# Kernel tuning notes

Hardware: AMD Instinct MI355X
Metric: run time of the kernel (lower is better)

## Reference

```python
import jax, jax.numpy as jnp
import numpy as np

N, C_IN, C_OUT, K_CHEB, BATCH = 2048, 64, 64, 4, 8


def setup_inputs() -> dict:
    key = jax.random.key(0)
    k1, k2, k3, k4, k5 = jax.random.split(key, 5)
    # Xavier-uniform-like scales
    s_nn = float(np.sqrt(6.0 / (N + N)))
    s_th = float(np.sqrt(6.0 / (C_IN + C_OUT)))
    return {
        "X": jax.random.normal(k1, (BATCH, N, C_IN), dtype=jnp.float32),
        "Ws": jax.random.uniform(k2, (N, N), jnp.float32, -s_nn, s_nn),
        "W_alpha": jax.random.uniform(k3, (N, N), jnp.float32, -s_nn, s_nn),
        "Theta_s": jax.random.uniform(k4, (K_CHEB, C_IN, C_OUT), jnp.float32, -s_th, s_th),
        "Theta_d": jax.random.uniform(k5, (K_CHEB, C_IN, C_OUT), jnp.float32, -s_th, s_th),
    }


def reference(X, Ws, W_alpha, Theta_s, Theta_d):
    B, n, c_in = X.shape
    K = Theta_s.shape[0]

    # ---- static filter: sum_k (T_k(Ws) @ X) @ Theta_s[k] ----
    # T_0 = I, so T_0 @ X = X
    static_filter = jnp.einsum('bni,io->bno', X, Theta_s[0])
    if K > 1:
        T_prev2 = jnp.eye(n, dtype=X.dtype)
        T_prev1 = Ws  # T_1
        for k in range(1, K):
            TkX = jnp.einsum('nm,bmi->bni', T_prev1, X)
            static_filter = static_filter + jnp.einsum('bni,io->bno', TkX, Theta_s[k])
            if k + 1 < K:  # incremental Chebyshev recursion (same values as from-scratch)
                T_prev2, T_prev1 = T_prev1, 2.0 * (Ws @ T_prev1) - T_prev2

    # ---- dynamic filter ----
    # Wd = X @ (W_alpha @ X)^T  -> [B, n, n]
    WaX = jnp.einsum('nm,bmi->bni', W_alpha, X)
    Wd = jnp.einsum('bni,bmi->bnm', X, WaX)

    dynamic_filter = jnp.einsum('bni,io->bno', X, Theta_d[0])
    if K > 1:
        Td_prev2 = jnp.broadcast_to(jnp.eye(n, dtype=X.dtype), (B, n, n))
        Td_prev1 = Wd  # T_1
        for k in range(1, K):
            TkX = jnp.einsum('bnm,bmi->bni', Td_prev1, X)
            dynamic_filter = dynamic_filter + jnp.einsum('bni,io->bno', TkX, Theta_d[k])
            if k + 1 < K:
                Td_prev2, Td_prev1 = Td_prev1, 2.0 * jnp.matmul(Wd, Td_prev1) - Td_prev2

    return jax.nn.relu(static_filter) + jax.nn.relu(dynamic_filter)
```

## Files before the change

### kernel.cpp

```cpp
#include <hip/hip_runtime.h>

typedef __attribute__((ext_vector_type(8))) short bf16x8;
typedef __attribute__((ext_vector_type(4))) float f32x4;

__device__ __forceinline__ ushort f32_to_bf16(float f) {
    union { float f; unsigned u; } v; v.f = f;
    unsigned b = v.u + 0x7FFF + ((v.u >> 16) & 1);
    return (ushort)(b >> 16);
}
__device__ __forceinline__ float bf16_to_f32(ushort h) {
    union { unsigned u; float f; } v; v.u = ((unsigned)h) << 16;
    return v.f;
}
__device__ __forceinline__ void split2(float x, ushort& a, ushort& b) {
    a = f32_to_bf16(x); float r1 = x - bf16_to_f32(a);
    b = f32_to_bf16(r1);
}

__device__ __forceinline__ void vmwait4() { asm volatile("s_waitcnt vmcnt(4)" ::: "memory"); }
__device__ __forceinline__ void vmwait0() { asm volatile("s_waitcnt vmcnt(0)" ::: "memory"); }
__device__ __forceinline__ void lgwait0() { asm volatile("s_waitcnt lgkmcnt(0)" ::: "memory"); }
__device__ __forceinline__ void blockbar() {
    __builtin_amdgcn_sched_barrier(0);
    __builtin_amdgcn_s_barrier();
    __builtin_amdgcn_sched_barrier(0);
}

__device__ __forceinline__ void stage64x64(const ushort* gsrc, int row_stride_elems,
                                           char* lds, int t256) {
    const char* gb = (const char*)gsrc;
    const int rs = row_stride_elems * 2;
#pragma unroll
    for (int j = 0; j < 2; ++j) {
        int o = (j * 256 + t256) * 16;
        int row = o >> 7;
        int col = (o & 127) ^ ((row & 7) << 4);
        __builtin_amdgcn_global_load_lds(
            (const __attribute__((address_space(1))) unsigned int*)(gb + row * rs + col),
            (__attribute__((address_space(3))) unsigned int*)(lds + o), 16, 0, 0);
    }
}

__device__ __forceinline__ bf16x8 fragld(const char* lds, int row, int kbyte) {
    return *(const bf16x8*)(lds + (row << 7) + (kbyte ^ ((row & 7) << 4)));
}

__global__ __launch_bounds__(256) void prep_all(const float* __restrict__ X,
        ushort* __restrict__ XT1, ushort* __restrict__ XT2,
        ushort* __restrict__ X1o, ushort* __restrict__ X2o,
        const float* __restrict__ Ws, ushort* __restrict__ Ws16,
        const float* __restrict__ Wa, ushort* __restrict__ Wa1, ushort* __restrict__ Wa2,
        const float* __restrict__ Ths, ushort* __restrict__ ThsT) {
    __shared__ float tile[64][68];
    const int bx = blockIdx.x;
    const int t = threadIdx.x;
    if (bx < 256) {
        const int b = bx >> 5, n0 = (bx & 31) * 64;
#pragma unroll
        for (int it = 0; it < 4; ++it) {
            int f = it * 256 + t, r = f >> 4, q = (f & 15) * 4;
            float4 v = *(const float4*)&X[((size_t)b * 2048 + n0 + r) * 64 + q];
            tile[r][q + 0] = v.x; tile[r][q + 1] = v.y; tile[r][q + 2] = v.z; tile[r][q + 3] = v.w;
        }
        __syncthreads();
#pragma unroll
        for (int it = 0; it < 4; ++it) {
            int f = it * 256 + t, c = f >> 4, q = (f & 15) * 4;
            ushort4 h1, h2;
            split2(tile[q + 0][c], h1.x, h2.x); split2(tile[q + 1][c], h1.y, h2.y);
            split2(tile[q + 2][c], h1.z, h2.z); split2(tile[q + 3][c], h1.w, h2.w);
            size_t a = (size_t)(b * 64 + c) * 2048 + n0 + q;
            *(ushort4*)&XT1[a] = h1; *(ushort4*)&XT2[a] = h2;
        }
#pragma unroll
        for (int it = 0; it < 4; ++it) {
            int f = it * 256 + t, n = f >> 4, q = (f & 15) * 4;
            ushort4 h1, h2;
            split2(tile[n][q + 0], h1.x, h2.x); split2(tile[n][q + 1], h1.y, h2.y);
            split2(tile[n][q + 2], h1.z, h2.z); split2(tile[n][q + 3], h1.w, h2.w);
            size_t a = (size_t)(n0 + n) * 512 + b * 64 + q;
            *(ushort4*)&X1o[a] = h1; *(ushort4*)&X2o[a] = h2;
        }
    } else if (bx < 2304) {
        size_t idx = ((size_t)(bx - 256) * 256 + t) * 8;
#pragma unroll
        for (int h = 0; h < 2; ++h) {
            float4 v = *(const float4*)&Ws[idx + h * 4];
            ushort4 a;
            a.x = f32_to_bf16(v.x); a.y = f32_to_bf16(v.y);
            a.z = f32_to_bf16(v.z); a.w = f32_to_bf16(v.w);
            *(ushort4*)&Ws16[idx + h * 4] = a;
        }
    } else if (bx < 4352) {
        size_t idx = ((size_t)(bx - 2304) * 256 + t) * 8;
#pragma unroll
        for (int h = 0; h < 2; ++h) {
            float4 v = *(const float4*)&Wa[idx + h * 4];
            ushort4 a, b;
            split2(v.x, a.x, b.x); split2(v.y, a.y, b.y);
            split2(v.z, a.z, b.z); split2(v.w, a.w, b.w);
            *(ushort4*)&Wa1[idx + h * 4] = a; *(ushort4*)&Wa2[idx + h * 4] = b;
        }
    } else {
        int idx = (bx - 4352) * 256 + t;
        int k = idx >> 12, o = (idx >> 6) & 63, i = idx & 63;
        ThsT[idx] = f32_to_bf16(Ths[k * 4096 + i * 64 + o]);
    }
}

template <int MODE>
__device__ __forceinline__ void gemm_s_body(int bx, const ushort* __restrict__ A,
        const ushort* __restrict__ BT, const ushort* __restrict__ CinT,
        ushort* __restrict__ YT, ushort* __restrict__ Yo, char* ls) {
    const int t = threadIdx.x;
    const int g = t >> 8, t256 = t & 255;
    const int m0 = (bx & 31) * 64, c0 = (bx >> 5) * 64;
    const int lane = t & 63;
    const int wg = (t >> 6) & 3, wr = wg >> 1, wc = wg & 1;
    const int l15 = lane & 15, l4 = lane >> 4;
    char* base = ls + g * 32768;
    const ushort* Ap = A + (size_t)m0 * 2048 + (size_t)g * 1024;
    const ushort* Bp = BT + (size_t)c0 * 2048 + (size_t)g * 1024;

    f32x4 z = {0.f, 0.f, 0.f, 0.f};
    f32x4 acc[2][2];
    acc[0][0] = z; acc[0][1] = z; acc[1][0] = z; acc[1][1] = z;

    stage64x64(Ap, 2048, base, t256);
    stage64x64(Bp, 2048, base + 8192, t256);
    for (int ts = 0; ts < 16; ++ts) {
        char* cur = base + (ts & 1) * 16384;
        if (ts < 15) {
            char* nxt = base + ((ts + 1) & 1) * 16384;
            stage64x64(Ap + (ts + 1) * 64, 2048, nxt, t256);
            stage64x64(Bp + (ts + 1) * 64, 2048, nxt + 8192, t256);
            vmwait4();
        } else {
            vmwait0();
        }
        blockbar();
#pragma unroll
        for (int s = 0; s < 2; ++s) {
            const int kb = s * 64 + l4 * 16;
            bf16x8 aF[2], bF[2];
#pragma unroll
            for (int f = 0; f < 2; ++f) {
                aF[f] = fragld(cur, wr * 32 + f * 16 + l15, kb);
                bF[f] = fragld(cur + 8192, wc * 32 + f * 16 + l15, kb);
            }
#pragma unroll
            for (int i = 0; i < 2; ++i)
#pragma unroll
                for (int j = 0; j < 2; ++j)
                    acc[i][j] = __builtin_amdgcn_mfma_f32_16x16x32_bf16(aF[i], bF[j], acc[i][j], 0, 0, 0);
        }
        lgwait0();
        blockbar();
    }

// ... 80 lines not shown
#pragma unroll
        for (int s = 0; s < 2; ++s) {
            const int kb = s * 64 + l4 * 16;
            bf16x8 aF[2], bF[2];
#pragma unroll
            for (int f = 0; f < 2; ++f) {
                aF[f] = fragld(cur, wr * 32 + f * 16 + l15, kb);
                bF[f] = fragld(cur + 8192, wc * 32 + f * 16 + l15, kb);
            }
#pragma unroll
            for (int i = 0; i < 2; ++i)
#pragma unroll
                for (int j = 0; j < 2; ++j)
                    acc[i][j] = __builtin_amdgcn_mfma_f32_16x16x32_bf16(aF[i], bF[j], acc[i][j], 0, 0, 0);
        }
        lgwait0();
        blockbar();
    }

    float* red = (float*)ls;
    float* tf = (float*)(ls + 17408);
    if (g == 0) {
#pragma unroll
        for (int i = 0; i < 2; ++i)
#pragma unroll
            for (int j = 0; j < 2; ++j) {
                const int lrb = wr * 32 + i * 16 + l4 * 4;
                const int lc = wc * 32 + j * 16 + l15;
#pragma unroll
                for (int r = 0; r < 4; ++r) red[(lrb + r) * 65 + lc] = acc[i][j][r];
            }
    }
    __syncthreads();
    if (g == 1) {
#pragma unroll
        for (int i = 0; i < 2; ++i)
#pragma unroll
            for (int j = 0; j < 2; ++j) {
                const int lrb = wr * 32 + i * 16 + l4 * 4;
                const int lc = wc * 32 + j * 16 + l15;
#pragma unroll
                for (int r = 0; r < 4; ++r) tf[(lrb + r) * 64 + lc] = red[(lrb + r) * 65 + lc] + acc[i][j][r];
            }
    }
    __syncthreads();
    {
        float* Pd = g2 ? P1 : P0;
        int row = t >> 3, q = (t & 7) * 8;
        *(float4*)&Pd[(size_t)(m0 + row) * 512 + c0 + q]     = *(float4*)&tf[row * 64 + q];
        *(float4*)&Pd[(size_t)(m0 + row) * 512 + c0 + q + 4] = *(float4*)&tf[row * 64 + q + 4];
    }
}

__device__ __forceinline__ void gemm3_body(int bx, const ushort* __restrict__ A1,
        const ushort* __restrict__ A2, const ushort* __restrict__ B1,
        const ushort* __restrict__ B2, float* __restrict__ WaXT, char* ls) {
    const int t = threadIdx.x;
    const int g = t >> 8, t256 = t & 255;
    const int m0 = (bx & 31) * 64, c0 = (bx >> 5) * 64;
    const int lane = t & 63;
    const int wg = (t >> 6) & 3, wr = wg >> 1, wc = wg & 1;
    const int l15 = lane & 15, l4 = lane >> 4;
    char* base = ls + g * 32768;
    const size_t kbase = (size_t)g * 1024;

    f32x4 z = {0.f, 0.f, 0.f, 0.f};
    f32x4 acc[2][2];
    acc[0][0] = z; acc[0][1] = z; acc[1][0] = z; acc[1][1] = z;

    for (int k0 = 0; k0 < 1024; k0 += 64) {
        stage64x64(A1 + (size_t)m0 * 2048 + kbase + k0, 2048, base + 0 * 8192, t256);
        stage64x64(A2 + (size_t)m0 * 2048 + kbase + k0, 2048, base + 1 * 8192, t256);
        stage64x64(B1 + (size_t)c0 * 2048 + kbase + k0, 2048, base + 2 * 8192, t256);
        stage64x64(B2 + (size_t)c0 * 2048 + kbase + k0, 2048, base + 3 * 8192, t256);
        __syncthreads();
#pragma unroll
        for (int s = 0; s < 2; ++s) {
            const int kb = s * 64 + l4 * 16;
            bf16x8 a1F[2], a2F[2], b1F[2], b2F[2];
#pragma unroll
            for (int f = 0; f < 2; ++f) {
                const int ar = wr * 32 + f * 16 + l15;
                const int br = wc * 32 + f * 16 + l15;
                a1F[f] = fragld(base + 0 * 8192, ar, kb);
                a2F[f] = fragld(base + 1 * 8192, ar, kb);
                b1F[f] = fragld(base + 2 * 8192, br, kb);
                b2F[f] = fragld(base + 3 * 8192, br, kb);
            }
#pragma unroll
            for (int i = 0; i < 2; ++i)
#pragma unroll
                for (int j = 0; j < 2; ++j) {
                    f32x4 a = acc[i][j];
                    a = __builtin_amdgcn_mfma_f32_16x16x32_bf16(a1F[i], b1F[j], a, 0, 0, 0);
                    a = __builtin_amdgcn_mfma_f32_16x16x32_bf16(a1F[i], b2F[j], a, 0, 0, 0);
                    a = __builtin_amdgcn_mfma_f32_16x16x32_bf16(a2F[i], b1F[j], a, 0, 0, 0);
                    acc[i][j] = a;
                }
        }
        __syncthreads();
    }

    float* red = (float*)ls;
    if (g == 0) {
#pragma unroll
        for (int i = 0; i < 2; ++i)
#pragma unroll
            for (int j = 0; j < 2; ++j) {
                const int lrb = wr * 32 + i * 16 + l4 * 4;
                const int lc = wc * 32 + j * 16 + l15;
#pragma unroll
                for (int r = 0; r < 4; ++r) red[(lrb + r) * 65 + lc] = acc[i][j][r];
            }
    }
    __syncthreads();
    if (g == 1) {
#pragma unroll
        for (int i = 0; i < 2; ++i)
#pragma unroll
            for (int j = 0; j < 2; ++j) {
                const int lrb = wr * 32 + i * 16 + l4 * 4;
                const int lc = wc * 32 + j * 16 + l15;
                f32x4 v;
#pragma unroll
                for (int r = 0; r < 4; ++r) v[r] = red[(lrb + r) * 65 + lc] + acc[i][j][r];
                *(f32x4*)&WaXT[(size_t)(c0 + lc) * 2048 + m0 + lrb] = v;
            }
    }
}

__device__ __forceinline__ void gram_body(int bx, const float* __restrict__ WaXT,
        const ushort* __restrict__ XT1, const ushort* __restrict__ XT2,
        float* __restrict__ Gpart, char* lsraw) {
    const int b = bx & 7, chunk = bx >> 3;
    float (*Lw)[68] = (float(*)[68])lsraw;
    float (*Rx)[68] = (float(*)[68])(lsraw + 64 * 68 * 4);
    const int t = threadIdx.x;
    const int n0 = chunk * 64;
    {
        const int r = t >> 3, q = (t & 7) * 8;
        size_t a = (size_t)(b * 64 + r) * 2048 + n0 + q;
        *(float4*)&Lw[r][q]     = *(const float4*)&WaXT[a];
        *(float4*)&Lw[r][q + 4] = *(const float4*)&WaXT[a + 4];
#pragma unroll
        for (int h = 0; h < 2; ++h) {
            ushort4 h1 = *(const ushort4*)&XT1[a + h * 4];
            ushort4 h2 = *(const ushort4*)&XT2[a + h * 4];
            Rx[r][q + h * 4 + 0] = bf16_to_f32(h1.x) + bf16_to_f32(h2.x);
            Rx[r][q + h * 4 + 1] = bf16_to_f32(h1.y) + bf16_to_f32(h2.y);
            Rx[r][q + h * 4 + 2] = bf16_to_f32(h1.z) + bf16_to_f32(h2.z);
            Rx[r][q + h * 4 + 3] = bf16_to_f32(h1.w) + bf16_to_f32(h2.w);
        }
    }
    __syncthreads();
    if (t < 256) {
        const int tx = t & 15, ty = t >> 4;
        float acc[4][4] = {{0.f,0.f,0.f,0.f},{0.f,0.f,0.f,0.f},{0.f,0.f,0.f,0.f},{0.f,0.f,0.f,0.f}};
        for (int n = 0; n < 64; ++n) {
            float a[4], bb[4];
#pragma unroll
            for (int i = 0; i < 4; ++i) { a[i] = Lw[ty * 4 + i][n]; bb[i] = Rx[tx * 4 + i][n]; }
#pragma unroll
            for (int i = 0; i < 4; ++i)
#pragma unroll
                for (int j = 0; j < 4; ++j) acc[i][j] = fmaf(a[i], bb[j], acc[i][j]);
        }
        float* gp = Gpart + (size_t)(chunk * 8 + b) * 4096;
#pragma unroll
        for (int i = 0; i < 4; ++i)
            *(float4*)&gp[(ty * 4 + i) * 64 + tx * 4] =
                make_float4(acc[i][0], acc[i][1], acc[i][2], acc[i][3]);
    }
}

__device__ __forceinline__ void cheb_body(int b, const float* __restrict__ Gpart,
        const float* __restrict__ Thd, ushort* __restrict__ DT1, ushort* __restrict__ DT2,
        char* lsraw) {
    float (*Gs)[68]  = (float(*)[68])lsraw;
    float (*C2s)[68] = (float(*)[68])(lsraw + 17408);
    float (*C3s)[68] = (float(*)[68])(lsraw + 34816);
    const int t = threadIdx.x;
    for (int i = t; i < 4096; i += 512) {
        float s = 0.f;
#pragma unroll
        for (int c = 0; c < 32; ++c) s += Gpart[((size_t)c * 8 + b) * 4096 + i];
        Gs[i >> 6][i & 63] = s;
    }
    __syncthreads();
    const int tx = t & 15, ty = (t >> 4) & 15;
    const int r0 = ty * 4, c0 = tx * 4;
    const bool act = t < 256;

    if (act) {
        float p[4][4] = {{0,0,0,0},{0,0,0,0},{0,0,0,0},{0,0,0,0}};
        for (int k = 0; k < 64; ++k) {
            float ar[4] = {Gs[r0][k], Gs[r0+1][k], Gs[r0+2][k], Gs[r0+3][k]};
            float4 bv = *(const float4*)&Gs[k][c0];
            float br[4] = {bv.x, bv.y, bv.z, bv.w};
#pragma unroll
            for (int i = 0; i < 4; ++i)
#pragma unroll
                for (int j = 0; j < 4; ++j) p[i][j] = fmaf(ar[i], br[j], p[i][j]);
        }
#pragma unroll
        for (int i = 0; i < 4; ++i)
#pragma unroll
            for (int j = 0; j < 4; ++j)
                C2s[r0+i][c0+j] = 2.f * p[i][j] - ((r0+i) == (c0+j) ? 1.f : 0.f);
    }
    __syncthreads();
    if (act) {
        float q[4][4] = {{0,0,0,0},{0,0,0,0},{0,0,0,0},{0,0,0,0}};
        for (int k = 0; k < 64; ++k) {
            float ar[4] = {Gs[r0][k], Gs[r0+1][k], Gs[r0+2][k], Gs[r0+3][k]};
            float4 bv = *(const float4*)&C2s[k][c0];
            float br[4] = {bv.x, bv.y, bv.z, bv.w};
#pragma unroll
            for (int i = 0; i < 4; ++i)
#pragma unroll
                for (int j = 0; j < 4; ++j) q[i][j] = fmaf(ar[i], br[j], q[i][j]);
        }
#pragma unroll
        for (int i = 0; i < 4; ++i)
#pragma unroll
            for (int j = 0; j < 4; ++j)
                C3s[r0+i][c0+j] = 2.f * q[i][j] - Gs[r0+i][c0+j];
    }
    __syncthreads();
    float d[4][4];
    if (act) {
#pragma unroll
        for (int i = 0; i < 4; ++i) {
            float4 t0 = *(const float4*)&Thd[(r0+i) * 64 + c0];
            d[i][0] = t0.x; d[i][1] = t0.y; d[i][2] = t0.z; d[i][3] = t0.w;
        }
        for (int k = 0; k < 64; ++k) {
            float4 t1 = *(const float4*)&Thd[4096 + k * 64 + c0];
            float4 t2 = *(const float4*)&Thd[8192 + k * 64 + c0];
            float4 t3 = *(const float4*)&Thd[12288 + k * 64 + c0];
            float a1[4] = {Gs[r0][k], Gs[r0+1][k], Gs[r0+2][k], Gs[r0+3][k]};
            float a2[4] = {C2s[r0][k], C2s[r0+1][k], C2s[r0+2][k], C2s[r0+3][k]};
            float a3[4] = {C3s[r0][k], C3s[r0+1][k], C3s[r0+2][k], C3s[r0+3][k]};
            float b1[4] = {t1.x, t1.y, t1.z, t1.w};
            float b2[4] = {t2.x, t2.y, t2.z, t2.w};
            float b3[4] = {t3.x, t3.y, t3.z, t3.w};
#pragma unroll
            for (int i = 0; i < 4; ++i)
#pragma unroll
                for (int j = 0; j < 4; ++j) {
                    d[i][j] = fmaf(a1[i], b1[j], d[i][j]);
                    d[i][j] = fmaf(a2[i], b2[j], d[i][j]);
                    d[i][j] = fmaf(a3[i], b3[j], d[i][j]);
                }
        }
    }
    __syncthreads();
    if (act) {
#pragma unroll
        for (int i = 0; i < 4; ++i)
#pragma unroll
            for (int j = 0; j < 4; ++j) Gs[r0 + i][c0 + j] = d[i][j];
    }
    __syncthreads();
    for (int it = 0; it < 8; ++it) {
        int idx = it * 512 + t;
        int o = idx >> 6, ii = idx & 63;
        ushort h1, h2;
        split2(Gs[ii][o], h1, h2);
        DT1[b * 4096 + idx] = h1;
        DT2[b * 4096 + idx] = h2;
    }
}

__global__ __launch_bounds__(512, 4) void mega1(const ushort* __restrict__ Wa1,
        const ushort* __restrict__ Wa2, const ushort* __restrict__ XT1,
        const ushort* __restrict__ XT2, float* __restrict__ WaXT,
        const ushort* __restrict__ Ws16, ushort* __restrict__ Y1T, ushort* __restrict__ Y1o) {
    __shared__ __align__(16) char ls[65536];
    const int bx = blockIdx.x;
    if (bx < 256) gemm3_body(bx, Wa1, Wa2, XT1, XT2, WaXT, ls);
    else          gemm_s_body<0>(bx - 256, Ws16, XT1, nullptr, Y1T, Y1o, ls);
}

__global__ __launch_bounds__(512, 4) void mega2(const ushort* __restrict__ Ws16,
        const ushort* __restrict__ Y1T, const ushort* __restrict__ XT1,
        ushort* __restrict__ Y2T, ushort* __restrict__ Y2o,
        const float* __restrict__ WaXT, const ushort* __restrict__ XT2,
        float* __restrict__ Gpart) {
    __shared__ __align__(16) char ls[65536];
    const int bx = blockIdx.x;
    if (bx < 256) gemm_s_body<1>(bx, Ws16, Y1T, XT1, Y2T, Y2o, ls);
    else          gram_body(bx - 256, WaXT, XT1, XT2, Gpart, ls);
}

__global__ __launch_bounds__(512, 4) void mega3(const ushort* __restrict__ Ws16,
        const ushort* __restrict__ Y2T, float* __restrict__ P0, float* __restrict__ P1,
        const float* __restrict__ Gpart, const float* __restrict__ Thd,
        ushort* __restrict__ DT1, ushort* __restrict__ DT2) {
    __shared__ __align__(16) char ls[65536];
    const int bx = blockIdx.x;
    if (bx < 512) y3_body(bx, Ws16, Y2T, P0, P1, ls);
    else          cheb_body(bx - 512, Gpart, Thd, DT1, DT2, ls);
}

__global__ __launch_bounds__(256) void ep_fused(const ushort* __restrict__ ThsT,
                                                const ushort* __restrict__ DT1, const ushort* __restrict__ DT2,
                                                const ushort* __restrict__ X1o, const ushort* __restrict__ X2o,
                                                const ushort* __restrict__ Y1o, const ushort* __restrict__ Y2o,
                                                const float* __restrict__ P0, const float* __restrict__ P1,
                                                float* __restrict__ out) {
    __shared__ __align__(16) char ls[65536];
    const int b = blockIdx.y, n0 = blockIdx.x * 64;
    const int t = threadIdx.x, lane = t & 63, w = t >> 6, wr = w >> 1, wc = w & 1;
    const int l15 = lane & 15, l4 = lane >> 4;

    const int r3 = t >> 2, q3e = (t & 3) * 16;
    const size_t a3 = (size_t)(n0 + r3) * 512 + b * 64 + q3e;
    float4 pA[4], pB[4];
    ushort4 y1v[4];
#pragma unroll
    for (int h = 0; h < 4; ++h) {
        pA[h]  = *(const float4*)&P0[a3 + h * 4];
        pB[h]  = *(const float4*)&P1[a3 + h * 4];
        y1v[h] = *(const ushort4*)&Y1o[a3 + h * 4];
    }

    stage64x64(X1o + (size_t)n0 * 512 + b * 64, 512, ls + 0 * 8192, t);
    stage64x64(Y1o + (size_t)n0 * 512 + b * 64, 512, ls + 1 * 8192, t);
    stage64x64(Y2o + (size_t)n0 * 512 + b * 64, 512, ls + 2 * 8192, t);
    stage64x64(ThsT + 0 * 4096, 64, ls + 4 * 8192, t);
    stage64x64(ThsT + 1 * 4096, 64, ls + 5 * 8192, t);
    stage64x64(ThsT + 2 * 4096, 64, ls + 6 * 8192, t);
    stage64x64(ThsT + 3 * 4096, 64, ls + 7 * 8192, t);
    {
        uint4 w0, w1;
        ushort* u0 = (ushort*)&w0;
        ushort* u1 = (ushort*)&w1;
#pragma unroll
        for (int h = 0; h < 2; ++h) {
            const float4 pa = pA[h], pb = pB[h];
            const ushort4 yv = y1v[h];
            u0[h * 4 + 0] = f32_to_bf16(2.f * (pa.x + pb.x) - bf16_to_f32(yv.x));
            u0[h * 4 + 1] = f32_to_bf16(2.f * (pa.y + pb.y) - bf16_to_f32(yv.y));
            u0[h * 4 + 2] = f32_to_bf16(2.f * (pa.z + pb.z) - bf16_to_f32(yv.z));
            u0[h * 4 + 3] = f32_to_bf16(2.f * (pa.w + pb.w) - bf16_to_f32(yv.w));
        }
#pragma unroll
        for (int h = 0; h < 2; ++h) {
            const float4 pa = pA[2 + h], pb = pB[2 + h];
            const ushort4 yv = y1v[2 + h];
            u1[h * 4 + 0] = f32_to_bf16(2.f * (pa.x + pb.x) - bf16_to_f32(yv.x));
            u1[h * 4 + 1] = f32_to_bf16(2.f * (pa.y + pb.y) - bf16_to_f32(yv.y));
            u1[h * 4 + 2] = f32_to_bf16(2.f * (pa.z + pb.z) - bf16_to_f32(yv.z));
            u1[h * 4 + 3] = f32_to_bf16(2.f * (pa.w + pb.w) - bf16_to_f32(yv.w));
        }
        const int bc0 = q3e * 2;
        const int sw = (r3 & 7) << 4;
        *(uint4*)(ls + 3 * 8192 + (r3 << 7) + ((bc0 + 0)  ^ sw)) = w0;
        *(uint4*)(ls + 3 * 8192 + (r3 << 7) + ((bc0 + 16) ^ sw)) = w1;
    }
    __syncthreads();

    f32x4 z = {0.f, 0.f, 0.f, 0.f};
    f32x4 as[2][2], ad[2][2];
    as[0][0] = z; as[0][1] = z; as[1][0] = z; as[1][1] = z;
    ad[0][0] = z; ad[0][1] = z; ad[1][0] = z; ad[1][1] = z;
#pragma unroll
    for (int s = 0; s < 2; ++s) {
        const int kb = s * 64 + l4 * 16;
#pragma unroll
        for (int p = 0; p < 4; ++p) {
            bf16x8 aF[2], bF[2];
#pragma unroll
            for (int f = 0; f < 2; ++f) {
                aF[f] = fragld(ls + (4 + p) * 8192, wr * 32 + f * 16 + l15, kb);
                bF[f] = fragld(ls + p * 8192, wc * 32 + f * 16 + l15, kb);
            }
#pragma unroll
            for (int i = 0; i < 2; ++i)
#pragma unroll
                for (int j = 0; j < 2; ++j)
                    as[i][j] = __builtin_amdgcn_mfma_f32_16x16x32_bf16(aF[i], bF[j], as[i][j], 0, 0, 0);
        }
    }
    __syncthreads();
    stage64x64(DT1 + b * 4096, 64, ls + 1 * 8192, t);
    stage64x64(DT2 + b * 4096, 64, ls + 2 * 8192, t);
    stage64x64(X2o + (size_t)n0 * 512 + b * 64, 512, ls + 3 * 8192, t);
    __syncthreads();
#pragma unroll
    for (int s = 0; s < 2; ++s) {
        const int kb = s * 64 + l4 * 16;
        bf16x8 a1[2], a2[2], b0[2], b3[2];
#pragma unroll
        for (int f = 0; f < 2; ++f) {
            a1[f] = fragld(ls + 1 * 8192, wr * 32 + f * 16 + l15, kb);
            a2[f] = fragld(ls + 2 * 8192, wr * 32 + f * 16 + l15, kb);
            b0[f] = fragld(ls + 0 * 8192, wc * 32 + f * 16 + l15, kb);
            b3[f] = fragld(ls + 3 * 8192, wc * 32 + f * 16 + l15, kb);
        }
#pragma unroll
        for (int i = 0; i < 2; ++i)
#pragma unroll
            for (int j = 0; j < 2; ++j) {
                f32x4 a = ad[i][j];
                a = __builtin_amdgcn_mfma_f32_16x16x32_bf16(a1[i], b0[j], a, 0, 0, 0);
                a = __builtin_amdgcn_mfma_f32_16x16x32_bf16(a1[i], b3[j], a, 0, 0, 0);
                a = __builtin_amdgcn_mfma_f32_16x16x32_bf16(a2[i], b0[j], a, 0, 0, 0);
                ad[i][j] = a;
            }
    }
#pragma unroll
    for (int i = 0; i < 2; ++i)
#pragma unroll
        for (int j = 0; j < 2; ++j) {
            const int ob = wr * 32 + i * 16 + l4 * 4;
            const int nn = wc * 32 + j * 16 + l15;
            float4 o4;
            o4.x = fmaxf(as[i][j][0], 0.f) + fmaxf(ad[i][j][0], 0.f);
            o4.y = fmaxf(as[i][j][1], 0.f) + fmaxf(ad[i][j][1], 0.f);
            o4.z = fmaxf(as[i][j][2], 0.f) + fmaxf(ad[i][j][2], 0.f);
            o4.w = fmaxf(as[i][j][3], 0.f) + fmaxf(ad[i][j][3], 0.f);
            *(float4*)&out[((size_t)b * 2048 + n0 + nn) * 64 + ob] = o4;
        }
}

extern "C" void kernel_launch(void* const* d_in, const int* in_sizes, int n_in,
                              void* d_out, int out_size, void* d_ws, size_t ws_size,
                              hipStream_t stream) {
    (void)in_sizes; (void)n_in; (void)out_size;
    const float* X   = (const float*)d_in[0];
    const float* Ws  = (const float*)d_in[1];
    const float* Wa  = (const float*)d_in[2];
    const float* Ths = (const float*)d_in[3];
    const float* Thd = (const float*)d_in[4];

    char* p = (char*)d_ws;
    auto alloc = [&](size_t bytes) { char* r = p; p += (bytes + 255) & ~(size_t)255; return r; };
    ushort* XT1 = (ushort*)alloc(512ull * 2048 * 2);
    ushort* XT2 = (ushort*)alloc(512ull * 2048 * 2);
    ushort* X1o = (ushort*)alloc(2048ull * 512 * 2);
    ushort* X2o = (ushort*)alloc(2048ull * 512 * 2);
    ushort* Ws16 = (ushort*)alloc(2048ull * 2048 * 2);
    ushort* Wa1 = (ushort*)alloc(2048ull * 2048 * 2);
    ushort* Wa2 = (ushort*)alloc(2048ull * 2048 * 2);
    ushort* Y1T = (ushort*)alloc(512ull * 2048 * 2);
    ushort* Y2T = (ushort*)alloc(512ull * 2048 * 2);
    ushort* Y1o = (ushort*)alloc(2048ull * 512 * 2);
    ushort* Y2o = (ushort*)alloc(2048ull * 512 * 2);
    float*  P0  = (float*)alloc(2048ull * 512 * 4);
    float*  P1  = (float*)alloc(2048ull * 512 * 4);
    float*  Gpart = (float*)alloc(32ull * 8 * 4096 * 4);
    ushort* DT1 = (ushort*)alloc(8ull * 4096 * 2);
    ushort* DT2 = (ushort*)alloc(8ull * 4096 * 2);
    ushort* ThsT = (ushort*)alloc(4ull * 4096 * 2);
    if ((size_t)(p - (char*)d_ws) > ws_size) return;
    float* WaXT = (float*)d_out;

    prep_all<<<4416, 256, 0, stream>>>(X, XT1, XT2, X1o, X2o, Ws, Ws16, Wa, Wa1, Wa2, Ths, ThsT);
    mega1<<<512, 512, 0, stream>>>(Wa1, Wa2, XT1, XT2, WaXT, Ws16, Y1T, Y1o);
    mega2<<<512, 512, 0, stream>>>(Ws16, Y1T, XT1, Y2T, Y2o, WaXT, XT2, Gpart);
    mega3<<<520, 512, 0, stream>>>(Ws16, Y2T, P0, P1, Gpart, Thd, DT1, DT2);
    ep_fused<<<dim3(32, 8), 256, 0, stream>>>(ThsT, DT1, DT2, X1o, X2o, Y1o, Y2o, P0, P1, (float*)d_out);
}
```

Baseline: 90.97 us.

## Rebalance work across fused kernels with split-K, interleaved roles, and smaller epilogue tiles

Splits the W_alpha·X GEMM into two K-halves written to separate partial buffers, and the gram stage sums them on load. This doubles the block count in mega1 and lets the X row-major split plus the Theta_s transpose move from the prep kernel into mega1 as a third block role. Block roles in mega1 and mega2 are interleaved so different work types share CUs. mega3 schedules the Chebyshev blocks first, the gram small-matmul now uses all 512 threads, and the epilogue uses 32-row tiles for twice as many blocks. The cost is extra workspace and global traffic for the partial sums, plus more complex indexing.

```diff
diff --git a/kernel.cpp b/kernel.cpp
--- a/kernel.cpp
+++ b/kernel.cpp
@@ -40,6 +40,17 @@
             (__attribute__((address_space(3))) unsigned int*)(lds + o), 16, 0, 0);
     }
 }
+__device__ __forceinline__ void stage32x64(const ushort* gsrc, int row_stride_elems,
+                                           char* lds, int t) {
+    const char* gb = (const char*)gsrc;
+    const int rs = row_stride_elems * 2;
+    int o = t * 16;
+    int row = o >> 7;
+    int col = (o & 127) ^ ((row & 7) << 4);
+    __builtin_amdgcn_global_load_lds(
+        (const __attribute__((address_space(1))) unsigned int*)(gb + row * rs + col),
+        (__attribute__((address_space(3))) unsigned int*)(lds + o), 16, 0, 0);
+}
 
 __device__ __forceinline__ bf16x8 fragld(const char* lds, int row, int kbyte) {
     return *(const bf16x8*)(lds + (row << 7) + (kbyte ^ ((row & 7) << 4)));
@@ -47,10 +58,8 @@
 
 __global__ __launch_bounds__(256) void prep_all(const float* __restrict__ X,
         ushort* __restrict__ XT1, ushort* __restrict__ XT2,
-        ushort* __restrict__ X1o, ushort* __restrict__ X2o,
         const float* __restrict__ Ws, ushort* __restrict__ Ws16,
-        const float* __restrict__ Wa, ushort* __restrict__ Wa1, ushort* __restrict__ Wa2,
-        const float* __restrict__ Ths, ushort* __restrict__ ThsT) {
+        const float* __restrict__ Wa, ushort* __restrict__ Wa1, ushort* __restrict__ Wa2) {
     __shared__ float tile[64][68];
     const int bx = blockIdx.x;
     const int t = threadIdx.x;
@@ -72,15 +81,6 @@
             size_t a = (size_t)(b * 64 + c) * 2048 + n0 + q;
             *(ushort4*)&XT1[a] = h1; *(ushort4*)&XT2[a] = h2;
         }
-#pragma unroll
-        for (int it = 0; it < 4; ++it) {
-            int f = it * 256 + t, n = f >> 4, q = (f & 15) * 4;
-            ushort4 h1, h2;
-            split2(tile[n][q + 0], h1.x, h2.x); split2(tile[n][q + 1], h1.y, h2.y);
-            split2(tile[n][q + 2], h1.z, h2.z); split2(tile[n][q + 3], h1.w, h2.w);
-            size_t a = (size_t)(n0 + n) * 512 + b * 64 + q;
-            *(ushort4*)&X1o[a] = h1; *(ushort4*)&X2o[a] = h2;
-        }
     } else if (bx < 2304) {
         size_t idx = ((size_t)(bx - 256) * 256 + t) * 8;
 #pragma unroll
@@ -91,7 +91,7 @@
             a.z = f32_to_bf16(v.z); a.w = f32_to_bf16(v.w);
             *(ushort4*)&Ws16[idx + h * 4] = a;
         }
-    } else if (bx < 4352) {
+    } else {
         size_t idx = ((size_t)(bx - 2304) * 256 + t) * 8;
 #pragma unroll
         for (int h = 0; h < 2; ++h) {
@@ -101,10 +101,37 @@
             split2(v.z, a.z, b.z); split2(v.w, a.w, b.w);
             *(ushort4*)&Wa1[idx + h * 4] = a; *(ushort4*)&Wa2[idx + h * 4] = b;
         }
-    } else {
-        int idx = (bx - 4352) * 256 + t;
-        int k = idx >> 12, o = (idx >> 6) & 63, i = idx & 63;
-        ThsT[idx] = f32_to_bf16(Ths[k * 4096 + i * 64 + o]);
+    }
+}
+
+__device__ __forceinline__ void xo_body(int idx, const float* __restrict__ X,
+        ushort* __restrict__ X1o, ushort* __restrict__ X2o,
+        const float* __restrict__ Ths, ushort* __restrict__ ThsT) {
+    const int t = threadIdx.x;
+    {
+        size_t e = ((size_t)idx * 512 + t) * 8;
+        int c0 = (int)(e & 63);
+        int n  = (int)((e >> 6) & 2047);
+        int b  = (int)(e >> 17);
+        float4 v0 = *(const float4*)&X[e];
+        float4 v1 = *(const float4*)&X[e + 4];
+        uint4 w1, w2;
+        ushort* u1 = (ushort*)&w1; ushort* u2 = (ushort*)&w2;
+        split2(v0.x, u1[0], u2[0]); split2(v0.y, u1[1], u2[1]);
+        split2(v0.z, u1[2], u2[2]); split2(v0.w, u1[3], u2[3]);
+        split2(v1.x, u1[4], u2[4]); split2(v1.y, u1[5], u2[5]);
+        split2(v1.z, u1[6], u2[6]); split2(v1.w, u1[7], u2[7]);
+        size_t dst = (size_t)n * 512 + b * 64 + c0;
+        *(uint4*)&X1o[dst] = w1;
+        *(uint4*)&X2o[dst] = w2;
+    }
+    if (idx < 8) {
+#pragma unroll
+        for (int k = 0; k < 4; ++k) {
+            int idx2 = idx * 512 + t + k * 4096;
+            int kk = idx2 >> 12, o = (idx2 >> 6) & 63, i = idx2 & 63;
+            ThsT[idx2] = f32_to_bf16(Ths[kk * 4096 + i * 64 + o]);
+        }
     }
 }
 
@@ -291,23 +318,25 @@
     }
 }
 
-__device__ __forceinline__ void gemm3_body(int bx, const ushort* __restrict__ A1,
+__device__ __forceinline__ void gemm3_body(int bxx, const ushort* __restrict__ A1,
         const ushort* __restrict__ A2, const ushort* __restrict__ B1,
-        const ushort* __restrict__ B2, float* __restrict__ WaXT, char* ls) {
+        const ushort* __restrict__ B2, float* __restrict__ WaXP0,
+        float* __restrict__ WaXP1, char* ls) {
     const int t = threadIdx.x;
     const int g = t >> 8, t256 = t & 255;
-    const int m0 = (bx & 31) * 64, c0 = (bx >> 5) * 64;
+    const int tile = bxx >> 1, g2 = bxx & 1;
+    const int m0 = (tile & 31) * 64, c0 = (tile >> 5) * 64;
     const int lane = t & 63;
     const int wg = (t >> 6) & 3, wr = wg >> 1, wc = wg & 1;
     const int l15 = lane & 15, l4 = lane >> 4;
     char* base = ls + g * 32768;
-    const size_t kbase = (size_t)g * 1024;
+    const size_t kbase = (size_t)g2 * 1024 + (size_t)g * 512;
 
     f32x4 z = {0.f, 0.f, 0.f, 0.f};
     f32x4 acc[2][2];
     acc[0][0] = z; acc[0][1] = z; acc[1][0] = z; acc[1][1] = z;
 
-    for (int k0 = 0; k0 < 1024; k0 += 64) {
+    for (int k0 = 0; k0 < 512; k0 += 64) {
         stage64x64(A1 + (size_t)m0 * 2048 + kbase + k0, 2048, base + 0 * 8192, t256);
         stage64x64(A2 + (size_t)m0 * 2048 + kbase + k0, 2048, base + 1 * 8192, t256);
         stage64x64(B1 + (size_t)c0 * 2048 + kbase + k0, 2048, base + 2 * 8192, t256);
@@ -354,6 +383,7 @@
     }
     __syncthreads();
     if (g == 1) {
+        float* Wd = g2 ? WaXP1 : WaXP0;
 #pragma unroll
         for (int i = 0; i < 2; ++i)
 #pragma unroll
@@ -363,15 +393,16 @@
                 f32x4 v;
 #pragma unroll
                 for (int r = 0; r < 4; ++r) v[r] = red[(lrb + r) * 65 + lc] + acc[i][j][r];
-                *(f32x4*)&WaXT[(size_t)(c0 + lc) * 2048 + m0 + lrb] = v;
-            }
-    }
-}
-
-__device__ __forceinline__ void gram_body(int bx, const float* __restrict__ WaXT,
+                *(f32x4*)&Wd[(size_t)(c0 + lc) * 2048 + m0 + lrb] = v;
+            }
+    }
+}
+
+__device__ __forceinline__ void gram_body(int idx, const float* __restrict__ WaXP0,
+        const float* __restrict__ WaXP1,
         const ushort* __restrict__ XT1, const ushort* __restrict__ XT2,
         float* __restrict__ Gpart, char* lsraw) {
-    const int b = bx & 7, chunk = bx >> 3;
+    const int b = idx & 7, chunk = idx >> 3;
     float (*Lw)[68] = (float(*)[68])lsraw;
     float (*Rx)[68] = (float(*)[68])(lsraw + 64 * 68 * 4);
     const int t = threadIdx.x;
@@ -379,8 +410,14 @@
     {
         const int r = t >> 3, q = (t & 7) * 8;
         size_t a = (size_t)(b * 64 + r) * 2048 + n0 + q;
-        *(float4*)&Lw[r][q]     = *(const float4*)&WaXT[a];
-        *(float4*)&Lw[r][q + 4] = *(const float4*)&WaXT[a + 4];
+        float4 w0a = *(const float4*)&WaXP0[a];
+        float4 w0b = *(const float4*)&WaXP0[a + 4];
+        float4 w1a = *(const float4*)&WaXP1[a];
+        float4 w1b = *(const float4*)&WaXP1[a + 4];
+        Lw[r][q + 0] = w0a.x + w1a.x; Lw[r][q + 1] = w0a.y + w1a.y;
+        Lw[r][q + 2] = w0a.z + w1a.z; Lw[r][q + 3] = w0a.w + w1a.w;
+        Lw[r][q + 4] = w0b.x + w1b.x; Lw[r][q + 5] = w0b.y + w1b.y;
+        Lw[r][q + 6] = w0b.z + w1b.z; Lw[r][q + 7] = w0b.w + w1b.w;
 #pragma unroll
         for (int h = 0; h < 2; ++h) {
             ushort4 h1 = *(const ushort4*)&XT1[a + h * 4];
@@ -426,80 +463,75 @@
         Gs[i >> 6][i & 63] = s;
     }
     __syncthreads();
-    const int tx = t & 15, ty = (t >> 4) & 15;
-    const int r0 = ty * 4, c0 = tx * 4;
-    const bool act = t < 256;
-
-    if (act) {
-        float p[4][4] = {{0,0,0,0},{0,0,0,0},{0,0,0,0},{0,0,0,0}};
+    const int tx = t & 15, ty = t >> 4;
+    const int r0 = ty * 2, c0 = tx * 4;
+    {
+        float p[2][4] = {{0,0,0,0},{0,0,0,0}};
         for (int k = 0; k < 64; ++k) {
-            float ar[4] = {Gs[r0][k], Gs[r0+1][k], Gs[r0+2][k], Gs[r0+3][k]};
+            float a0 = Gs[r0][k], a1 = Gs[r0 + 1][k];
             float4 bv = *(const float4*)&Gs[k][c0];
-            float br[4] = {bv.x, bv.y, bv.z, bv.w};
-#pragma unroll
-            for (int i = 0; i < 4; ++i)
-#pragma unroll
-                for (int j = 0; j < 4; ++j) p[i][j] = fmaf(ar[i], br[j], p[i][j]);
-        }
-#pragma unroll
-        for (int i = 0; i < 4; ++i)
+            p[0][0] = fmaf(a0, bv.x, p[0][0]); p[0][1] = fmaf(a0, bv.y, p[0][1]);
+            p[0][2] = fmaf(a0, bv.z, p[0][2]); p[0][3] = fmaf(a0, bv.w, p[0][3]);
+            p[1][0] = fmaf(a1, bv.x, p[1][0]); p[1][1] = fmaf(a1, bv.y, p[1][1]);
+            p[1][2] = fmaf(a1, bv.z, p[1][2]); p[1][3] = fmaf(a1, bv.w, p[1][3]);
+        }
+#pragma unroll
+        for (int i = 0; i < 2; ++i)
 #pragma unroll
             for (int j = 0; j < 4; ++j)
-                C2s[r0+i][c0+j] = 2.f * p[i][j] - ((r0+i) == (c0+j) ? 1.f : 0.f);
-    }
-    __syncthreads();
-    if (act) {
-        float q[4][4] = {{0,0,0,0},{0,0,0,0},{0,0,0,0},{0,0,0,0}};
+                C2s[r0 + i][c0 + j] = 2.f * p[i][j] - ((r0 + i) == (c0 + j) ? 1.f : 0.f);
+    }
+    __syncthreads();
+    {
+        float q[2][4] = {{0,0,0,0},{0,0,0,0}};
         for (int k = 0; k < 64; ++k) {
-            float ar[4] = {Gs[r0][k], Gs[r0+1][k], Gs[r0+2][k], Gs[r0+3][k]};
+            float a0 = Gs[r0][k], a1 = Gs[r0 + 1][k];
             float4 bv = *(const float4*)&C2s[k][c0];
-            float br[4] = {bv.x, bv.y, bv.z, bv.w};
-#pragma unroll
-            for (int i = 0; i < 4; ++i)
-#pragma unroll
-                for (int j = 0; j < 4; ++j) q[i][j] = fmaf(ar[i], br[j], q[i][j]);
-        }
-#pragma unroll
-        for (int i = 0; i < 4; ++i)
+            q[0][0] = fmaf(a0, bv.x, q[0][0]); q[0][1] = fmaf(a0, bv.y, q[0][1]);
+            q[0][2] = fmaf(a0, bv.z, q[0][2]); q[0][3] = fmaf(a0, bv.w, q[0][3]);
+            q[1][0] = fmaf(a1, bv.x, q[1][0]); q[1][1] = fmaf(a1, bv.y, q[1][1]);
+            q[1][2] = fmaf(a1, bv.z, q[1][2]); q[1][3] = fmaf(a1, bv.w, q[1][3]);
+        }
+#pragma unroll
+        for (int i = 0; i < 2; ++i)
 #pragma unroll
             for (int j = 0; j < 4; ++j)
-                C3s[r0+i][c0+j] = 2.f * q[i][j] - Gs[r0+i][c0+j];
-    }
-    __syncthreads();
-    float d[4][4];
-    if (act) {
-#pragma unroll
-        for (int i = 0; i < 4; ++i) {
-            float4 t0 = *(const float4*)&Thd[(r0+i) * 64 + c0];
+                C3s[r0 + i][c0 + j] = 2.f * q[i][j] - Gs[r0 + i][c0 + j];
+    }
+    __syncthreads();
+    float d[2][4];
+    {
+#pragma unroll
+        for (int i = 0; i < 2; ++i) {
+            float4 t0 = *(const float4*)&Thd[(r0 + i) * 64 + c0];
             d[i][0] = t0.x; d[i][1] = t0.y; d[i][2] = t0.z; d[i][3] = t0.w;
         }
         for (int k = 0; k < 64; ++k) {
             float4 t1 = *(const float4*)&Thd[4096 + k * 64 + c0];
             float4 t2 = *(const float4*)&Thd[8192 + k * 64 + c0];
             float4 t3 = *(const float4*)&Thd[12288 + k * 64 + c0];
-            float a1[4] = {Gs[r0][k], Gs[r0+1][k], Gs[r0+2][k], Gs[r0+3][k]};
-            float a2[4] = {C2s[r0][k], C2s[r0+1][k], C2s[r0+2][k], C2s[r0+3][k]};
-            float a3[4] = {C3s[r0][k], C3s[r0+1][k], C3s[r0+2][k], C3s[r0+3][k]};
-            float b1[4] = {t1.x, t1.y, t1.z, t1.w};
-            float b2[4] = {t2.x, t2.y, t2.z, t2.w};
-            float b3[4] = {t3.x, t3.y, t3.z, t3.w};
-#pragma unroll
-            for (int i = 0; i < 4; ++i)
-#pragma unroll
-                for (int j = 0; j < 4; ++j) {
-                    d[i][j] = fmaf(a1[i], b1[j], d[i][j]);
-                    d[i][j] = fmaf(a2[i], b2[j], d[i][j]);
-                    d[i][j] = fmaf(a3[i], b3[j], d[i][j]);
-                }
-        }
-    }
-    __syncthreads();
-    if (act) {
-#pragma unroll
-        for (int i = 0; i < 4; ++i)
-#pragma unroll
-            for (int j = 0; j < 4; ++j) Gs[r0 + i][c0 + j] = d[i][j];
-    }
+            float g0 = Gs[r0][k], g1 = Gs[r0 + 1][k];
+            float c20 = C2s[r0][k], c21 = C2s[r0 + 1][k];
+            float c30 = C3s[r0][k], c31 = C3s[r0 + 1][k];
+            d[0][0] = fmaf(g0, t1.x, d[0][0]); d[0][1] = fmaf(g0, t1.y, d[0][1]);
+            d[0][2] = fmaf(g0, t1.z, d[0][2]); d[0][3] = fmaf(g0, t1.w, d[0][3]);
+            d[1][0] = fmaf(g1, t1.x, d[1][0]); d[1][1] = fmaf(g1, t1.y, d[1][1]);
+            d[1][2] = fmaf(g1, t1.z, d[1][2]); d[1][3] = fmaf(g1, t1.w, d[1][3]);
+            d[0][0] = fmaf(c20, t2.x, d[0][0]); d[0][1] = fmaf(c20, t2.y, d[0][1]);
+            d[0][2] = fmaf(c20, t2.z, d[0][2]); d[0][3] = fmaf(c20, t2.w, d[0][3]);
+            d[1][0] = fmaf(c21, t2.x, d[1][0]); d[1][1] = fmaf(c21, t2.y, d[1][1]);
+            d[1][2] = fmaf(c21, t2.z, d[1][2]); d[1][3] = fmaf(c21, t2.w, d[1][3]);
+            d[0][0] = fmaf(c30, t3.x, d[0][0]); d[0][1] = fmaf(c30, t3.y, d[0][1]);
+            d[0][2] = fmaf(c30, t3.z, d[0][2]); d[0][3] = fmaf(c30, t3.w, d[0][3]);
+            d[1][0] = fmaf(c31, t3.x, d[1][0]); d[1][1] = fmaf(c31, t3.y, d[1][1]);
+            d[1][2] = fmaf(c31, t3.z, d[1][2]); d[1][3] = fmaf(c31, t3.w, d[1][3]);
+        }
+    }
+    __syncthreads();
+#pragma unroll
+    for (int i = 0; i < 2; ++i)
+#pragma unroll
+        for (int j = 0; j < 4; ++j) Gs[r0 + i][c0 + j] = d[i][j];
     __syncthreads();
     for (int it = 0; it < 8; ++it) {
         int idx = it * 512 + t;
@@ -513,23 +545,28 @@
 
 __global__ __launch_bounds__(512, 4) void mega1(const ushort* __restrict__ Wa1,
         const ushort* __restrict__ Wa2, const ushort* __restrict__ XT1,
-        const ushort* __restrict__ XT2, float* __restrict__ WaXT,
-        const ushort* __restrict__ Ws16, ushort* __restrict__ Y1T, ushort* __restrict__ Y1o) {
+        const ushort* __restrict__ XT2, float* __restrict__ WaXP0, float* __restrict__ WaXP1,
+        const ushort* __restrict__ Ws16, ushort* __restrict__ Y1T, ushort* __restrict__ Y1o,
+        const float* __restrict__ X, ushort* __restrict__ X1o, ushort* __restrict__ X2o,
+        const float* __restrict__ Ths, ushort* __restrict__ ThsT) {
     __shared__ __align__(16) char ls[65536];
     const int bx = blockIdx.x;
-    if (bx < 256) gemm3_body(bx, Wa1, Wa2, XT1, XT2, WaXT, ls);
-    else          gemm_s_body<0>(bx - 256, Ws16, XT1, nullptr, Y1T, Y1o, ls);
+    const int role = bx & 3, idx = bx >> 2;
+    if (role <= 1)      gemm3_body(idx * 2 + role, Wa1, Wa2, XT1, XT2, WaXP0, WaXP1, ls);
+    else if (role == 2) gemm_s_body<0>(idx, Ws16, XT1, nullptr, Y1T, Y1o, ls);
+    else                xo_body(idx, X, X1o, X2o, Ths, ThsT);
 }
 
 __global__ __launch_bounds__(512, 4) void mega2(const ushort* __restrict__ Ws16,
         const ushort* __restrict__ Y1T, const ushort* __restrict__ XT1,
         ushort* __restrict__ Y2T, ushort* __restrict__ Y2o,
-        const float* __restrict__ WaXT, const ushort* __restrict__ XT2,
-        float* __restrict__ Gpart) {
+        const float* __restrict__ WaXP0, const float* __restrict__ WaXP1,
+        const ushort* __restrict__ XT2, float* __restrict__ Gpart) {
     __shared__ __align__(16) char ls[65536];
     const int bx = blockIdx.x;
-    if (bx < 256) gemm_s_body<1>(bx, Ws16, Y1T, XT1, Y2T, Y2o, ls);
-    else          gram_body(bx - 256, WaXT, XT1, XT2, Gpart, ls);
+    const int role = bx & 1, idx = bx >> 1;
+    if (role == 0) gemm_s_body<1>(idx, Ws16, Y1T, XT1, Y2T, Y2o, ls);
+    else           gram_body(idx, WaXP0, WaXP1, XT1, XT2, Gpart, ls);
 }
 
 __global__ __launch_bounds__(512, 4) void mega3(const ushort* __restrict__ Ws16,
@@ -538,8 +575,8 @@
         ushort* __restrict__ DT1, ushort* __restrict__ DT2) {
     __shared__ __align__(16) char ls[65536];
     const int bx = blockIdx.x;
-    if (bx < 512) y3_body(bx, Ws16, Y2T, P0, P1, ls);
-    else          cheb_body(bx - 512, Gpart, Thd, DT1, DT2, ls);
+    if (bx < 8) cheb_body(bx, Gpart, Thd, DT1, DT2, ls);
+    else        y3_body(bx - 8, Ws16, Y2T, P0, P1, ls);
 }
 
 __global__ __launch_bounds__(256) void ep_fused(const ushort* __restrict__ ThsT,
@@ -548,120 +585,90 @@
                                                 const ushort* __restrict__ Y1o, const ushort* __restrict__ Y2o,
                                                 const float* __restrict__ P0, const float* __restrict__ P1,
                                                 float* __restrict__ out) {
-    __shared__ __align__(16) char ls[65536];
-    const int b = blockIdx.y, n0 = blockIdx.x * 64;
-    const int t = threadIdx.x, lane = t & 63, w = t >> 6, wr = w >> 1, wc = w & 1;
+    __shared__ __align__(16) char ls[49152];
+    const int b = blockIdx.y, n0 = blockIdx.x * 32;
+    const int t = threadIdx.x, lane = t & 63, w = t >> 6, wr = w & 1, wc = w >> 1;
     const int l15 = lane & 15, l4 = lane >> 4;
 
-    const int r3 = t >> 2, q3e = (t & 3) * 16;
-    const size_t a3 = (size_t)(n0 + r3) * 512 + b * 64 + q3e;
-    float4 pA[4], pB[4];
-    ushort4 y1v[4];
-#pragma unroll
-    for (int h = 0; h < 4; ++h) {
-        pA[h]  = *(const float4*)&P0[a3 + h * 4];
-        pB[h]  = *(const float4*)&P1[a3 + h * 4];
-        y1v[h] = *(const ushort4*)&Y1o[a3 + h * 4];
-    }
-
-    stage64x64(X1o + (size_t)n0 * 512 + b * 64, 512, ls + 0 * 8192, t);
-    stage64x64(Y1o + (size_t)n0 * 512 + b * 64, 512, ls + 1 * 8192, t);
-    stage64x64(Y2o + (size_t)n0 * 512 + b * 64, 512, ls + 2 * 8192, t);
-    stage64x64(ThsT + 0 * 4096, 64, ls + 4 * 8192, t);
-    stage64x64(ThsT + 1 * 4096, 64, ls + 5 * 8192, t);
-    stage64x64(ThsT + 2 * 4096, 64, ls + 6 * 8192, t);
-    stage64x64(ThsT + 3 * 4096, 64, ls + 7 * 8192, t);
+    const int r3 = t >> 3, q3 = (t & 7) * 8;
+    const size_t a3 = (size_t)(n0 + r3) * 512 + b * 64 + q3;
+    float4 p0a = *(const float4*)&P0[a3];
+    float4 p0b = *(const float4*)&P0[a3 + 4];
+    float4 p1a = *(const float4*)&P1[a3];
+    float4 p1b = *(const float4*)&P1[a3 + 4];
+    ushort4 y1a = *(const ushort4*)&Y1o[a3];
+    ushort4 y1b = *(const ushort4*)&Y1o[a3 + 4];
+
+    stage32x64(X1o + (size_t)n0 * 512 + b * 64, 512, ls + 0 * 4096, t);
+    stage32x64(Y1o + (size_t)n0 * 512 + b * 64, 512, ls + 1 * 4096, t);
+    stage32x64(Y2o + (size_t)n0 * 512 + b * 64, 512, ls + 2 * 4096, t);
+    stage64x64(ThsT + 0 * 4096, 64, ls + 16384 + 0 * 8192, t);
+    stage64x64(ThsT + 1 * 4096, 64, ls + 16384 + 1 * 8192, t);
+    stage64x64(ThsT + 2 * 4096, 64, ls + 16384 + 2 * 8192, t);
+    stage64x64(ThsT + 3 * 4096, 64, ls + 16384 + 3 * 8192, t);
     {
-        uint4 w0, w1;
-        ushort* u0 = (ushort*)&w0;
-        ushort* u1 = (ushort*)&w1;
-#pragma unroll
-        for (int h = 0; h < 2; ++h) {
-            const float4 pa = pA[h], pb = pB[h];
-            const ushort4 yv = y1v[h];
-            u0[h * 4 + 0] = f32_to_bf16(2.f * (pa.x + pb.x) - bf16_to_f32(yv.x));
-            u0[h * 4 + 1] = f32_to_bf16(2.f * (pa.y + pb.y) - bf16_to_f32(yv.y));
-            u0[h * 4 + 2] = f32_to_bf16(2.f * (pa.z + pb.z) - bf16_to_f32(yv.z));
-            u0[h * 4 + 3] = f32_to_bf16(2.f * (pa.w + pb.w) - bf16_to_f32(yv.w));
-        }
-#pragma unroll
-        for (int h = 0; h < 2; ++h) {
-            const float4 pa = pA[2 + h], pb = pB[2 + h];
-            const ushort4 yv = y1v[2 + h];
-            u1[h * 4 + 0] = f32_to_bf16(2.f * (pa.x + pb.x) - bf16_to_f32(yv.x));
-            u1[h * 4 + 1] = f32_to_bf16(2.f * (pa.y + pb.y) - bf16_to_f32(yv.y));
-            u1[h * 4 + 2] = f32_to_bf16(2.f * (pa.z + pb.z) - bf16_to_f32(yv.z));
-            u1[h * 4 + 3] = f32_to_bf16(2.f * (pa.w + pb.w) - bf16_to_f32(yv.w));
-        }
-        const int bc0 = q3e * 2;
-        const int sw = (r3 & 7) << 4;
-        *(uint4*)(ls + 3 * 8192 + (r3 << 7) + ((bc0 + 0)  ^ sw)) = w0;
-        *(uint4*)(ls + 3 * 8192 + (r3 << 7) + ((bc0 + 16) ^ sw)) = w1;
+        uint4 wv;
+        ushort* u = (ushort*)&wv;
+        u[0] = f32_to_bf16(2.f * (p0a.x + p1a.x) - bf16_to_f32(y1a.x));
+        u[1] = f32_to_bf16(2.f * (p0a.y + p1a.y) - bf16_to_f32(y1a.y));
+        u[2] = f32_to_bf16(2.f * (p0a.z + p1a.z) - bf16_to_f32(y1a.z));
+        u[3] = f32_to_bf16(2.f * (p0a.w + p1a.w) - bf16_to_f32(y1a.w));
+        u[4] = f32_to_bf16(2.f * (p0b.x + p1b.x) - bf16_to_f32(y1b.x));
+        u[5] = f32_to_bf16(2.f * (p0b.y + p1b.y) - bf16_to_f32(y1b.y));
+        u[6] = f32_to_bf16(2.f * (p0b.z + p1b.z) - bf16_to_f32(y1b.z));
+        u[7] = f32_to_bf16(2.f * (p0b.w + p1b.w) - bf16_to_f32(y1b.w));
+        *(uint4*)(ls + 3 * 4096 + (r3 << 7) + ((q3 * 2) ^ ((r3 & 7) << 4))) = wv;
     }
     __syncthreads();
 
     f32x4 z = {0.f, 0.f, 0.f, 0.f};
-    f32x4 as[2][2], ad[2][2];
-    as[0][0] = z; as[0][1] = z; as[1][0] = z; as[1][1] = z;
-    ad[0][0] = z; ad[0][1] = z; ad[1][0] = z; ad[1][1] = z;
+    f32x4 as[2], ad[2];
+    as[0] = z; as[1] = z; ad[0] = z; ad[1] = z;
 #pragma unroll
     for (int s = 0; s < 2; ++s) {
         const int kb = s * 64 + l4 * 16;
 #pragma unroll
         for (int p = 0; p < 4; ++p) {
-            bf16x8 aF[2], bF[2];
-#pragma unroll
-            for (int f = 0; f < 2; ++f) {
-                aF[f] = fragld(ls + (4 + p) * 8192, wr * 32 + f * 16 + l15, kb);
-                bF[f] = fragld(ls + p * 8192, wc * 32 + f * 16 + l15, kb);
-            }
-#pragma unroll
-            for (int i = 0; i < 2; ++i)
-#pragma unroll
-                for (int j = 0; j < 2; ++j)
-                    as[i][j] = __builtin_amdgcn_mfma_f32_16x16x32_bf16(aF[i], bF[j], as[i][j], 0, 0, 0);
-        }
-    }
-    __syncthreads();
-    stage64x64(DT1 + b * 4096, 64, ls + 1 * 8192, t);
-    stage64x64(DT2 + b * 4096, 64, ls + 2 * 8192, t);
-    stage64x64(X2o + (size_t)n0 * 512 + b * 64, 512, ls + 3 * 8192, t);
+            bf16x8 bF = fragld(ls + p * 4096, wc * 16 + l15, kb);
+#pragma unroll
+            for (int i = 0; i < 2; ++i) {
+                bf16x8 aF = fragld(ls + 16384 + p * 8192, wr * 32 + i * 16 + l15, kb);
+                as[i] = __builtin_amdgcn_mfma_f32_16x16x32_bf16(aF, bF, as[i], 0, 0, 0);
+            }
+        }
+    }
+    __syncthreads();
+    stage64x64(DT1 + b * 4096, 64, ls + 16384 + 0 * 8192, t);
+    stage64x64(DT2 + b * 4096, 64, ls + 16384 + 1 * 8192, t);
+    stage32x64(X2o + (size_t)n0 * 512 + b * 64, 512, ls + 3 * 4096, t);
     __syncthreads();
 #pragma unroll
     for (int s = 0; s < 2; ++s) {
         const int kb = s * 64 + l4 * 16;
-        bf16x8 a1[2], a2[2], b0[2], b3[2];
-#pragma unroll
-        for (int f = 0; f < 2; ++f) {
-            a1[f] = fragld(ls + 1 * 8192, wr * 32 + f * 16 + l15, kb);
-            a2[f] = fragld(ls + 2 * 8192, wr * 32 + f * 16 + l15, kb);
-            b0[f] = fragld(ls + 0 * 8192, wc * 32 + f * 16 + l15, kb);
-            b3[f] = fragld(ls + 3 * 8192, wc * 32 + f * 16 + l15, kb);
-        }
-#pragma unroll
-        for (int i = 0; i < 2; ++i)
-#pragma unroll
-            for (int j = 0; j < 2; ++j) {
-                f32x4 a = ad[i][j];
-                a = __builtin_amdgcn_mfma_f32_16x16x32_bf16(a1[i], b0[j], a, 0, 0, 0);
-                a = __builtin_amdgcn_mfma_f32_16x16x32_bf16(a1[i], b3[j], a, 0, 0, 0);
-                a = __builtin_amdgcn_mfma_f32_16x16x32_bf16(a2[i], b0[j], a, 0, 0, 0);
-                ad[i][j] = a;
-            }
-    }
-#pragma unroll
-    for (int i = 0; i < 2; ++i)
-#pragma unroll
-        for (int j = 0; j < 2; ++j) {
-            const int ob = wr * 32 + i * 16 + l4 * 4;
-            const int nn = wc * 32 + j * 16 + l15;
-            float4 o4;
-            o4.x = fmaxf(as[i][j][0], 0.f) + fmaxf(ad[i][j][0], 0.f);
-            o4.y = fmaxf(as[i][j][1], 0.f) + fmaxf(ad[i][j][1], 0.f);
-            o4.z = fmaxf(as[i][j][2], 0.f) + fmaxf(ad[i][j][2], 0.f);
-            o4.w = fmaxf(as[i][j][3], 0.f) + fmaxf(ad[i][j][3], 0.f);
-            *(float4*)&out[((size_t)b * 2048 + n0 + nn) * 64 + ob] = o4;
-        }
+        bf16x8 b0 = fragld(ls + 0 * 4096, wc * 16 + l15, kb);
+        bf16x8 b3 = fragld(ls + 3 * 4096, wc * 16 + l15, kb);
+#pragma unroll
+        for (int i = 0; i < 2; ++i) {
+            bf16x8 a1 = fragld(ls + 16384 + 0 * 8192, wr * 32 + i * 16 + l15, kb);
+            bf16x8 a2 = fragld(ls + 16384 + 1 * 8192, wr * 32 + i * 16 + l15, kb);
+            f32x4 a = ad[i];
+            a = __builtin_amdgcn_mfma_f32_16x16x32_bf16(a1, b0, a, 0, 0, 0);
+            a = __builtin_amdgcn_mfma_f32_16x16x32_bf16(a1, b3, a, 0, 0, 0);
+            a = __builtin_amdgcn_mfma_f32_16x16x32_bf16(a2, b0, a, 0, 0, 0);
+            ad[i] = a;
+        }
+    }
+#pragma unroll
+    for (int i = 0; i < 2; ++i) {
+        const int ob = wr * 32 + i * 16 + l4 * 4;
+        const int nn = wc * 16 + l15;
+        float4 o4;
+        o4.x = fmaxf(as[i][0], 0.f) + fmaxf(ad[i][0], 0.f);
+        o4.y = fmaxf(as[i][1], 0.f) + fmaxf(ad[i][1], 0.f);
+        o4.z = fmaxf(as[i][2], 0.f) + fmaxf(ad[i][2], 0.f);
+        o4.w = fmaxf(as[i][3], 0.f) + fmaxf(ad[i][3], 0.f);
+        *(float4*)&out[((size_t)b * 2048 + n0 + nn) * 64 + ob] = o4;
+    }
 }
 
 extern "C" void kernel_launch(void* const* d_in, const int* in_sizes, int n_in,
@@ -689,16 +696,18 @@
     ushort* Y2o = (ushort*)alloc(2048ull * 512 * 2);
     float*  P0  = (float*)alloc(2048ull * 512 * 4);
     float*  P1  = (float*)alloc(2048ull * 512 * 4);
+    float*  WaXP0 = (float*)alloc(512ull * 2048 * 4);
+    float*  WaXP1 = (float*)alloc(512ull * 2048 * 4);
     float*  Gpart = (float*)alloc(32ull * 8 * 4096 * 4);
     ushort* DT1 = (ushort*)alloc(8ull * 4096 * 2);
     ushort* DT2 = (ushort*)alloc(8ull * 4096 * 2);
     ushort* ThsT = (ushort*)alloc(4ull * 4096 * 2);
     if ((size_t)(p - (char*)d_ws) > ws_size) return;
-    float* WaXT = (float*)d_out;
-
-    prep_all<<<4416, 256, 0, stream>>>(X, XT1, XT2, X1o, X2o, Ws, Ws16, Wa, Wa1, Wa2, Ths, ThsT);
-    mega1<<<512, 512, 0, stream>>>(Wa1, Wa2, XT1, XT2, WaXT, Ws16, Y1T, Y1o);
-    mega2<<<512, 512, 0, stream>>>(Ws16, Y1T, XT1, Y2T, Y2o, WaXT, XT2, Gpart);
+
+    prep_all<<<4352, 256, 0, stream>>>(X, XT1, XT2, Ws, Ws16, Wa, Wa1, Wa2);
+    mega1<<<1024, 512, 0, stream>>>(Wa1, Wa2, XT1, XT2, WaXP0, WaXP1, Ws16, Y1T, Y1o,
+                                    X, X1o, X2o, Ths, ThsT);
+    mega2<<<512, 512, 0, stream>>>(Ws16, Y1T, XT1, Y2T, Y2o, WaXP0, WaXP1, XT2, Gpart);
     mega3<<<520, 512, 0, stream>>>(Ws16, Y2T, P0, P1, Gpart, Thd, DT1, DT2);
-    ep_fused<<<dim3(32, 8), 256, 0, stream>>>(ThsT, DT1, DT2, X1o, X2o, Y1o, Y2o, P0, P1, (float*)d_out);
-}
+    ep_fused<<<dim3(64, 8), 256, 0, stream>>>(ThsT, DT1, DT2, X1o, X2o, Y1o, Y2o, P0, P1, (float*)d_out);
+}
```

Result: slower. 99.00 us (+8.8%).
